# Kernel tuning notes

Measured on AMD Instinct MI355X. Metric: run time of the kernel, lower is better.

The kernel has to match this reference:

```python
import jax, jax.numpy as jnp
import numpy as np

NUM_HEADS = 8


def setup_inputs() -> dict:
    key = jax.random.key(0)
    ks = jax.random.split(key, 7)
    b, t, prompt_dim, emb_dim = 2, 4096, 256, 512
    hidden = emb_dim  # head_dim=None -> hidden_dim = emb_dim
    def xavier(k, fan_in, fan_out):
        limit = np.sqrt(6.0 / (fan_in + fan_out)).astype(np.float32)
        return jax.random.uniform(k, (fan_in, fan_out), jnp.float32, -limit, limit)
    return {
        "prompt": jax.random.normal(ks[0], (b, t, prompt_dim), jnp.float32),
        "Wp": xavier(ks[1], prompt_dim, emb_dim),
        "bp": jnp.zeros((emb_dim,), jnp.float32),
        "Wqkv": xavier(ks[2], emb_dim, 3 * hidden),
        "bqkv": jnp.zeros((3 * hidden,), jnp.float32),
        "Wo": xavier(ks[3], hidden, prompt_dim),
        "bo": jnp.zeros((prompt_dim,), jnp.float32),
    }


def reference(prompt, Wp, bp, Wqkv, bqkv, Wo, bo):
    # prompt_proj
    x = prompt @ Wp + bp                      # [b, t, emb_dim]
    b, t, c = x.shape
    qkv = x @ Wqkv + bqkv                     # [b, t, 3*hidden]
    q, k, v = jnp.split(qkv, 3, axis=2)
    def to_heads(z):
        return z.reshape(b, t, NUM_HEADS, -1).transpose(0, 2, 1, 3)  # [b, h, t, d]
    q, k, v = to_heads(q), to_heads(k), to_heads(v)
    d = k.shape[-1]
    scores = jnp.einsum("bhid,bhjd->bhij", q, k) / jnp.sqrt(jnp.float32(d))
    attn = jax.nn.softmax(scores, axis=-1)    # dropout = identity (eval)
    out = jnp.einsum("bhij,bhjd->bhid", attn, v)
    out = out.transpose(0, 2, 1, 3).reshape(b, t, -1)  # [b, t, hidden]
    return out @ Wo + bo                      # [b, t, prompt_dim]
```

## Files before the change

### kernel.cpp

```cpp
#include <hip/hip_runtime.h>
#include <math.h>
#include <stdint.h>


typedef unsigned short u16;
typedef __attribute__((ext_vector_type(8))) __bf16 bf16x8;
typedef __attribute__((ext_vector_type(4))) __bf16 bf16x4;
typedef __attribute__((ext_vector_type(4))) float f32x4;

#define AS1 __attribute__((address_space(1)))
#define AS3 __attribute__((address_space(3)))

__device__ __forceinline__ void async16(const void* g, void* l) {
  __builtin_amdgcn_global_load_lds((const AS1 void*)g, (AS3 void*)l, 16, 0, 0);
}

__device__ __forceinline__ u16 f2bf(float f) {
  union { float f; unsigned u; } c; c.f = f;
  return (u16)((c.u + 0x7fffu + ((c.u >> 16) & 1u)) >> 16);
}

__global__ void prep_kernel(const float* __restrict__ prompt, u16* __restrict__ pbf,
                            const float* __restrict__ Wp, const float* __restrict__ Wqkv,
                            const float* __restrict__ Wo, u16* __restrict__ woT,
                            const float* __restrict__ bp, const float* __restrict__ bqkv,
                            float* __restrict__ bfused, u16* __restrict__ wfT) {
  __shared__ u16 Asf[64 * 40];
  __shared__ u16 Bsf[64 * 32];
  __shared__ float red[256];
  const int bid = blockIdx.x, tid = threadIdx.x;
  if (bid < 96) {
    const int k0 = (bid & 3) * 64, n0 = (bid >> 2) * 64;
    const int lane = tid & 63, w = tid >> 6;
    const int wr = w >> 1, wc = w & 1;
    const int lr = lane >> 4, lc = lane & 15;
    f32x4 acc[2][2];
#pragma unroll
    for (int a = 0; a < 2; a++)
#pragma unroll
      for (int b = 0; b < 2; b++) acc[a][b] = (f32x4){0.f, 0.f, 0.f, 0.f};
    for (int e0 = 0; e0 < 512; e0 += 32) {
      {
        const int er = tid >> 3, ng = (tid & 7) * 8;
        float4 v1 = *(const float4*)&Wqkv[(e0 + er) * 1536 + n0 + ng];
        float4 v2 = *(const float4*)&Wqkv[(e0 + er) * 1536 + n0 + ng + 4];
        Asf[(ng + 0) * 40 + er] = f2bf(v1.x); Asf[(ng + 1) * 40 + er] = f2bf(v1.y);
        Asf[(ng + 2) * 40 + er] = f2bf(v1.z); Asf[(ng + 3) * 40 + er] = f2bf(v1.w);
        Asf[(ng + 4) * 40 + er] = f2bf(v2.x); Asf[(ng + 5) * 40 + er] = f2bf(v2.y);
        Asf[(ng + 6) * 40 + er] = f2bf(v2.z); Asf[(ng + 7) * 40 + er] = f2bf(v2.w);
      }
      {
        const int kr = tid >> 2, ec = (tid & 3) * 8;
        float4 w1 = *(const float4*)&Wp[(k0 + kr) * 512 + e0 + ec];
        float4 w2 = *(const float4*)&Wp[(k0 + kr) * 512 + e0 + ec + 4];
        u16 tmp[8] = {f2bf(w1.x), f2bf(w1.y), f2bf(w1.z), f2bf(w1.w),
                      f2bf(w2.x), f2bf(w2.y), f2bf(w2.z), f2bf(w2.w)};
        *(uint4*)&Bsf[kr * 32 + ec] = *(const uint4*)&tmp[0];
      }
      __syncthreads();
      bf16x8 af[2], bf2[2];
#pragma unroll
      for (int mi = 0; mi < 2; mi++)
        af[mi] = *(const bf16x8*)&Asf[(wr * 32 + mi * 16 + lc) * 40 + lr * 8];
#pragma unroll
      for (int nj = 0; nj < 2; nj++)
        bf2[nj] = *(const bf16x8*)&Bsf[(wc * 32 + nj * 16 + lc) * 32 + lr * 8];
#pragma unroll
      for (int mi = 0; mi < 2; mi++)
#pragma unroll
        for (int nj = 0; nj < 2; nj++)
          acc[mi][nj] = __builtin_amdgcn_mfma_f32_16x16x32_bf16(af[mi], bf2[nj], acc[mi][nj], 0, 0, 0);
      __syncthreads();
    }
#pragma unroll
    for (int mi = 0; mi < 2; mi++)
#pragma unroll
      for (int nj = 0; nj < 2; nj++)
#pragma unroll
        for (int r = 0; r < 4; r++)
          wfT[(n0 + wr * 32 + mi * 16 + 4 * lr + r) * 256 + k0 + wc * 32 + nj * 16 + lc] =
              f2bf(acc[mi][nj][r]);
  } else if (bid < 120) {
    const int nloc = tid & 63, slice = tid >> 6;
    const int n = (bid - 96) * 64 + nloc;
    float s = 0.f;
#pragma unroll 8
    for (int e = slice * 128; e < slice * 128 + 128; e++) s += bp[e] * Wqkv[e * 1536 + n];
    red[tid] = s;
    __syncthreads();
    if (slice == 0)
      bfused[n] = red[nloc] + red[64 + nloc] + red[128 + nloc] + red[192 + nloc] + bqkv[n];
  } else if (bid < 632) {
    int j = (bid - 120) * 256 + tid;
    int n = j >> 9, k = j & 511;
    woT[j] = f2bf(Wo[k * 256 + n]);
  } else {
    int i = (bid - 632) * 256 + tid;
    float4 v = ((const float4*)prompt)[i];
    ushort4 o;
    o.x = f2bf(v.x); o.y = f2bf(v.y); o.z = f2bf(v.z); o.w = f2bf(v.w);
    ((ushort4*)pbf)[i] = o;
  }
}

__global__ __launch_bounds__(256) void gemm_qkv(
    const u16* __restrict__ A, const u16* __restrict__ Bt, const float* __restrict__ bias,
    u16* __restrict__ qO, u16* __restrict__ kO, u16* __restrict__ vO, int K) {
  constexpr int MI = 4, NJ = 4;
  __shared__ __align__(16) u16 SH[16896];
  const int tid = threadIdx.x;
  const int lane = tid & 63, w = tid >> 6;
  const int wr = w >> 1, wc = w & 1;
  const int lr = lane >> 4, lc = lane & 15;
  const long tileM = (long)blockIdx.y * 128;
  const long tileN = (long)blockIdx.x * 128;

  f32x4 acc[MI][NJ];
#pragma unroll
  for (int a = 0; a < MI; a++)
#pragma unroll
    for (int b = 0; b < NJ; b++) acc[a][b] = (f32x4){0.f, 0.f, 0.f, 0.f};

  const int r0 = lane >> 2;
  const int blk = lane & 3;

  auto stage = [&](int buf, int k0) {
#pragma unroll
    for (int i = 0; i < 2; i++) {
      int r = w * 32 + i * 16 + r0;
      int g = (blk ^ ((r >> 1) & 3)) << 3;
      async16(A + (tileM + r) * (long)K + k0 + g,
              (void*)&SH[buf * 4096 + (w * 32 + i * 16) * 32]);
      async16(Bt + (tileN + r) * (long)K + k0 + g,
              (void*)&SH[8192 + buf * 4096 + (w * 32 + i * 16) * 32]);
    }
  };

  stage(0, 0);
  for (int k0 = 0; k0 < K; k0 += 32) {
    const int cur = (k0 >> 5) & 1;
    stage(cur ^ 1, (k0 + 32 < K) ? k0 + 32 : 0);
    asm volatile("s_waitcnt vmcnt(4)" ::: "memory");
    asm volatile("s_barrier" ::: "memory");

    bf16x8 af[MI], bfv[NJ];
#pragma unroll
    for (int mi = 0; mi < MI; mi++) {
      int r = wr * 64 + mi * 16 + lc;
      af[mi] = *(const bf16x8*)&SH[cur * 4096 + r * 32 + ((lr ^ ((r >> 1) & 3)) << 3)];
    }
#pragma unroll
    for (int nj = 0; nj < NJ; nj++) {
      int r = wc * 64 + nj * 16 + lc;
      bfv[nj] = *(const bf16x8*)&SH[8192 + cur * 4096 + r * 32 + ((lr ^ ((r >> 1) & 3)) << 3)];
    }
#pragma unroll
    for (int mi = 0; mi < MI; mi++)
#pragma unroll
      for (int nj = 0; nj < NJ; nj++)
        acc[mi][nj] = __builtin_amdgcn_mfma_f32_16x16x32_bf16(af[mi], bfv[nj], acc[mi][nj], 0, 0, 0);
    asm volatile("s_barrier" ::: "memory");
  }

  asm volatile("s_waitcnt vmcnt(0)" ::: "memory");
  __syncthreads();

  const int sec = (int)(tileN >> 9);
  const int bb = (int)(tileM >> 12);
  const int t0b = (int)(tileM & 4095);
  const int h0 = ((int)(tileN & 511)) >> 6;
  const float sc = (sec == 0) ? 0.18033688f : 1.f;

#pragma unroll
  for (int mi = 0; mi < MI; mi++)
#pragma unroll
    for (int nj = 0; nj < NJ; nj++) {
      int nloc = wc * 64 + nj * 16 + lc;
      float bcol = bias[tileN + nloc];
      int m0 = wr * 64 + mi * 16 + lr * 4;
      int p0 = m0;
      if (sec == 2) {
        int gg = (m0 >> 2) & 7;
        int posg = ((gg & 3) << 1) | (gg >> 2);
        p0 = (m0 & ~31) | (posg << 2);
      }
      u16 tmp[4];
#pragma unroll
      for (int r = 0; r < 4; r++) tmp[r] = f2bf((acc[mi][nj][r] + bcol) * sc);
      *(uint2*)&SH[nloc * 132 + p0] = *(const uint2*)&tmp[0];
    }
  __syncthreads();

  if (sec == 2) {
    const int rsub = tid >> 4;
    const int cch = tid & 15;
#pragma unroll
    for (int i = 0; i < 8; i++) {
      int row = i * 16 + rsub;
      int hh = row >> 6, d = row & 63;
      bf16x8 vv = *(const bf16x8*)&SH[row * 132 + cch * 8];
      long pl = bb * 8 + h0 + hh;
      *(bf16x8*)&vO[(pl * 64 + d) * 4096 + t0b + cch * 8] = vv;
    }
  } else {
    u16* dst = sec ? kO : qO;
    const int dgrp = lane & 7;
    const int msub = lane >> 3;
#pragma unroll
    for (int hh = 0; hh < 2; hh++) {
      long pl = bb * 8 + h0 + hh;
#pragma unroll
      for (int i = 0; i < 4; i++) {
        int m = w * 8 + msub + i * 32;
        u16 pk[8];
#pragma unroll
        for (int j = 0; j < 8; j++)
          pk[j] = SH[(hh * 64 + dgrp * 8 + j) * 132 + m];
        *(uint4*)&dst[((pl * 4096 + t0b + m) << 6) + dgrp * 8] = *(const uint4*)&pk[0];
      }
    }
  }
}

__global__ __launch_bounds__(512, 4) void flash_attn(
    const u16* __restrict__ Q, const u16* __restrict__ Kg,
    const u16* __restrict__ VTg, u16* __restrict__ Op, float* __restrict__ lp) {
  __shared__ __align__(16) u16 KV[2][8192];

  const int tid = threadIdx.x, lane = tid & 63, w = tid >> 6;
  const int linear = blockIdx.x + 16 * (blockIdx.y + 16 * blockIdx.z);
  const int qt = linear >> 5;
  const int g = linear & 31;
  const int plane = g & 15;
  const int split = g >> 4;
  const int lr = lane >> 4, lc = lane & 15;
  const long pbase = (long)plane << 18;
  const int qr0 = qt * 256 + w * 32;
  const int tj0 = split * 32;

  bf16x8 bq[2][2];
#pragma unroll
  for (int qi = 0; qi < 2; qi++)
#pragma unroll
    for (int kk = 0; kk < 2; kk++)
      bq[qi][kk] = *(const bf16x8*)&Q[pbase + (long)(qr0 + qi * 16 + lc) * 64 + kk * 32 + lr * 8];

  bf16x8 ones;
#pragma unroll
  for (int u = 0; u < 8; u++) ones[u] = (__bf16)1.0f;
  const f32x4 zero4 = (f32x4){0.f, 0.f, 0.f, 0.f};

  f32x4 o[2][4], o1[2];
#pragma unroll
  for (int mi = 0; mi < 2; mi++) {
    o1[mi] = zero4;
#pragma unroll
    for (int nj = 0; nj < 4; nj++) o[mi][nj] = zero4;
  }

  const int krow = lane >> 3, kblk = lane & 7;

  auto stage = [&](int buf, int tj) {
    const u16* kS = Kg + pbase + (long)tj * 4096;
    const u16* vS = VTg + pbase + (long)tj * 64;
    int row = w * 8 + krow;
    async16(kS + (long)row * 64 + ((kblk ^ (row & 7)) << 3),
            (void*)&KV[buf][(w * 8) * 64]);
    async16(vS + (long)row * 4096 + ((kblk ^ (row & 7)) << 3),
            (void*)&KV[buf][4096 + (w * 8) * 64]);
  };

  stage(0, tj0);
  for (int j = 0; j < 32; j++) {
    const int cur = j & 1;
    stage(cur ^ 1, (j + 1 < 32) ? tj0 + j + 1 : tj0);
    asm volatile("s_waitcnt vmcnt(2)" ::: "memory");
    asm volatile("s_barrier" ::: "memory");

    const u16* Ks = &KV[cur][0];
    const u16* Vt = &KV[cur][4096];

    f32x4 s[4][2];
#pragma unroll
    for (int ki = 0; ki < 4; ki++) {
      const int row = ki * 16 + lc;
      bf16x8 ak[2];
#pragma unroll
      for (int kk = 0; kk < 2; kk++)
        ak[kk] = *(const bf16x8*)&Ks[row * 64 + (((kk * 4 + lr) ^ (row & 7)) << 3)];
#pragma unroll
      for (int qi = 0; qi < 2; qi++) {
        s[ki][qi] = __builtin_amdgcn_mfma_f32_16x16x32_bf16(ak[0], bq[qi][0], zero4, 0, 0, 0);
        s[ki][qi] = __builtin_amdgcn_mfma_f32_16x16x32_bf16(ak[1], bq[qi][1], s[ki][qi], 0, 0, 0);
      }
    }

#pragma unroll
    for (int kk = 0; kk < 2; kk++) {
      bf16x8 ap[2];
#pragma unroll
      for (int qi = 0; qi < 2; qi++) {
        bf16x8 p;
#pragma unroll
        for (int r = 0; r < 4; r++) {
          p[r]     = (__bf16)__builtin_amdgcn_exp2f(s[2 * kk][qi][r]);
          p[4 + r] = (__bf16)__builtin_amdgcn_exp2f(s[2 * kk + 1][qi][r]);
        }
        ap[qi] = p;
      }
#pragma unroll
      for (int nj = 0; nj < 4; nj++) {
        const int row = nj * 16 + lc;
        bf16x8 bv = *(const bf16x8*)&Vt[row * 64 + (((kk * 4 + lr) ^ (row & 7)) << 3)];
#pragma unroll
        for (int mi = 0; mi < 2; mi++)
          o[mi][nj] = __builtin_amdgcn_mfma_f32_16x16x32_bf16(ap[mi], bv, o[mi][nj], 0, 0, 0);
      }
#pragma unroll
      for (int mi = 0; mi < 2; mi++)
        o1[mi] = __builtin_amdgcn_mfma_f32_16x16x32_bf16(ap[mi], ones, o1[mi], 0, 0, 0);
    }
    asm volatile("s_barrier" ::: "memory");
  }

  const int bb = plane >> 3, h = plane & 7;
  u16* Ob = Op + (long)split * 4194304;
#pragma unroll
  for (int mi = 0; mi < 2; mi++)
#pragma unroll
    for (int r = 0; r < 4; r++) {
      long t = qr0 + mi * 16 + 4 * lr + r;
#pragma unroll
      for (int nj = 0; nj < 4; nj++)
        Ob[(((long)(bb * 4096 + t) * 8 + h) << 6) + nj * 16 + lc] = f2bf(o[mi][nj][r]);
      if (lc == 0) lp[((split * 16 + plane) << 12) + t] = o1[mi][r];
    }
}

__global__ __launch_bounds__(256) void gemm_out(
    const u16* __restrict__ Op, const float* __restrict__ lp,
    const u16* __restrict__ Bt, const float* __restrict__ bias,
    float* __restrict__ outf) {
  constexpr int K = 512;
  __shared__ __align__(16) u16 As[2][64 * 32];
  __shared__ __align__(16) u16 Bs[2][64 * 32];
  const int tid = threadIdx.x;
  const int lane = tid & 63, w = tid >> 6;
  const int wr = w >> 1, wc = w & 1;
  const int lr = lane >> 4, lc = lane & 15;
  const long tileM = (long)blockIdx.y * 64;
  const long tileN = (long)blockIdx.x * 64;

  f32x4 acc[2][2];
#pragma unroll
  for (int a = 0; a < 2; a++)
#pragma unroll
    for (int b = 0; b < 2; b++) acc[a][b] = (f32x4){0.f, 0.f, 0.f, 0.f};

  const int r0 = lane >> 2;
  const int blk = lane & 3;

  auto stageB = [&](int buf, int k0) {
    int r = w * 16 + r0;
    int g = (blk ^ ((r >> 1) & 3)) << 3;
    async16(Bt + (tileN + r) * (long)K + k0 + g, (void*)&Bs[buf][(w * 16) * 32]);
  };

  const int ar = tid >> 2, ablk = tid & 3;
  const long arow = tileM + ar;
  const int ab = (int)(arow >> 12), at = (int)(arow & 4095);

  auto stageA = [&](int buf, int k0) {
    int h = k0 >> 6;
    float l = lp[(long)((ab * 8 + h) << 12) + at] +
              lp[(long)((16 + ab * 8 + h) << 12) + at];
    float inv = 1.f / l;
    long idx = arow * 512 + k0 + ablk * 8;
    bf16x8 v0 = *(const bf16x8*)&Op[idx];
    bf16x8 v1 = *(const bf16x8*)&Op[4194304 + idx];
    u16 tmp[8];
#pragma unroll
    for (int e = 0; e < 8; e++)
      tmp[e] = f2bf(((float)v0[e] + (float)v1[e]) * inv);
    *(uint4*)&As[buf][ar * 32 + ((ablk ^ ((ar >> 1) & 3)) << 3)] = *(const uint4*)&tmp[0];
  };

  stageB(0, 0);
  for (int k0 = 0; k0 < K; k0 += 32) {
    const int cur = (k0 >> 5) & 1;
    stageB(cur ^ 1, (k0 + 32 < K) ? k0 + 32 : 0);
    stageA(cur, k0);
    asm volatile("s_waitcnt vmcnt(1) lgkmcnt(0)" ::: "memory");
    asm volatile("s_barrier" ::: "memory");

    bf16x8 af[2], bfv[2];
#pragma unroll
    for (int mi = 0; mi < 2; mi++) {
      int r = wr * 32 + mi * 16 + lc;
      af[mi] = *(const bf16x8*)&As[cur][r * 32 + ((lr ^ ((r >> 1) & 3)) << 3)];
    }
#pragma unroll
    for (int nj = 0; nj < 2; nj++) {
      int r = wc * 32 + nj * 16 + lc;
      bfv[nj] = *(const bf16x8*)&Bs[cur][r * 32 + ((lr ^ ((r >> 1) & 3)) << 3)];
    }
#pragma unroll
    for (int mi = 0; mi < 2; mi++)
#pragma unroll
      for (int nj = 0; nj < 2; nj++)
        acc[mi][nj] = __builtin_amdgcn_mfma_f32_16x16x32_bf16(af[mi], bfv[nj], acc[mi][nj], 0, 0, 0);
    asm volatile("s_barrier" ::: "memory");
  }

#pragma unroll
  for (int mi = 0; mi < 2; mi++)
#pragma unroll
    for (int nj = 0; nj < 2; nj++) {
      long col = tileN + wc * 32 + nj * 16 + lc;
      float bcol = bias[col];
      long row0 = tileM + wr * 32 + mi * 16 + lr * 4;
#pragma unroll
      for (int r = 0; r < 4; r++)
        outf[(row0 + r) * 256 + col] = acc[mi][nj][r] + bcol;
    }
}

extern "C" void kernel_launch(void* const* d_in, const int* in_sizes, int n_in,
                              void* d_out, int out_size, void* d_ws, size_t ws_size,
                              hipStream_t stream) {
  const float* prompt = (const float*)d_in[0];
  const float* Wp = (const float*)d_in[1];
  const float* bp = (const float*)d_in[2];
  const float* Wqkv = (const float*)d_in[3];
  const float* bqkv = (const float*)d_in[4];
  const float* Wo = (const float*)d_in[5];
  const float* bo = (const float*)d_in[6];
  float* out = (float*)d_out;

  char* ws = (char*)d_ws;
  const size_t MiB = 1024 * 1024;
  u16* qb     = (u16*)(ws + 0);
  u16* kb     = (u16*)(ws + 8 * MiB);
  u16* vb     = (u16*)(ws + 16 * MiB);
  u16* pbf    = (u16*)(ws + 24 * MiB);
  float* lpp  = (float*)(ws + 24 * MiB);
  u16* Op     = (u16*)(ws + 28 * MiB);
  u16* woT    = (u16*)(ws + 44 * MiB);
  u16* wfT    = (u16*)(ws + 44 * MiB + 256 * 1024);
  float* bfused = (float*)(ws + 45 * MiB);

  prep_kernel<<<dim3(2680), dim3(256), 0, stream>>>(
      prompt, pbf, Wp, Wqkv, Wo, woT, bp, bqkv, bfused, wfT);

  gemm_qkv<<<dim3(12, 64), dim3(256), 0, stream>>>(
      pbf, wfT, bfused, qb, kb, vb, 256);

  flash_attn<<<dim3(16, 16, 2), dim3(512), 0, stream>>>(qb, kb, vb, Op, lpp);

  gemm_out<<<dim3(4, 128), dim3(256), 0, stream>>>(Op, lpp, woT, bo, out);
}
```

Baseline: 176.0 us.

## Fuse prompt bf16 conversion into QKV GEMM and register-prefetch A tiles

Removes the separate prompt fp32-to-bf16 pass from the prep kernel. The QKV GEMM now reads fp32 prompt rows directly into registers, converts them and writes them to LDS one iteration ahead. The output GEMM likewise splits its A staging into a register prefetch (load) and a later convert/write, so global latency overlaps the MFMA work. This cuts a full write and re-read of the bf16 prompt buffer, at the cost of more registers and twice the A-side global bytes inside the GEMM.

```diff
diff --git a/kernel.cpp b/kernel.cpp
--- a/kernel.cpp
+++ b/kernel.cpp
@@ -20,8 +20,7 @@
   return (u16)((c.u + 0x7fffu + ((c.u >> 16) & 1u)) >> 16);
 }
 
-__global__ void prep_kernel(const float* __restrict__ prompt, u16* __restrict__ pbf,
-                            const float* __restrict__ Wp, const float* __restrict__ Wqkv,
+__global__ void prep_kernel(const float* __restrict__ Wp, const float* __restrict__ Wqkv,
                             const float* __restrict__ Wo, u16* __restrict__ woT,
                             const float* __restrict__ bp, const float* __restrict__ bqkv,
                             float* __restrict__ bfused, u16* __restrict__ wfT) {
@@ -90,21 +89,15 @@
     __syncthreads();
     if (slice == 0)
       bfused[n] = red[nloc] + red[64 + nloc] + red[128 + nloc] + red[192 + nloc] + bqkv[n];
-  } else if (bid < 632) {
+  } else {
     int j = (bid - 120) * 256 + tid;
     int n = j >> 9, k = j & 511;
     woT[j] = f2bf(Wo[k * 256 + n]);
-  } else {
-    int i = (bid - 632) * 256 + tid;
-    float4 v = ((const float4*)prompt)[i];
-    ushort4 o;
-    o.x = f2bf(v.x); o.y = f2bf(v.y); o.z = f2bf(v.z); o.w = f2bf(v.w);
-    ((ushort4*)pbf)[i] = o;
   }
 }
 
 __global__ __launch_bounds__(256) void gemm_qkv(
-    const u16* __restrict__ A, const u16* __restrict__ Bt, const float* __restrict__ bias,
+    const float* __restrict__ Ap, const u16* __restrict__ Bt, const float* __restrict__ bias,
     u16* __restrict__ qO, u16* __restrict__ kO, u16* __restrict__ vO, int K) {
   constexpr int MI = 4, NJ = 4;
   __shared__ __align__(16) u16 SH[16896];
@@ -124,23 +117,45 @@
   const int r0 = lane >> 2;
   const int blk = lane & 3;
 
-  auto stage = [&](int buf, int k0) {
+  auto stageB = [&](int buf, int k0) {
 #pragma unroll
     for (int i = 0; i < 2; i++) {
       int r = w * 32 + i * 16 + r0;
       int g = (blk ^ ((r >> 1) & 3)) << 3;
-      async16(A + (tileM + r) * (long)K + k0 + g,
-              (void*)&SH[buf * 4096 + (w * 32 + i * 16) * 32]);
       async16(Bt + (tileN + r) * (long)K + k0 + g,
               (void*)&SH[8192 + buf * 4096 + (w * 32 + i * 16) * 32]);
     }
   };
 
-  stage(0, 0);
+  float4 aLo[2], aHi[2];
+  auto loadA = [&](int k0) {
+#pragma unroll
+    for (int i = 0; i < 2; i++) {
+      int r = w * 32 + i * 16 + r0;
+      int gch = blk ^ ((r >> 1) & 3);
+      const float* src = &Ap[(tileM + r) * 256 + k0 + gch * 8];
+      aLo[i] = *(const float4*)src;
+      aHi[i] = *(const float4*)(src + 4);
+    }
+  };
+  auto writeA = [&](int buf) {
+#pragma unroll
+    for (int i = 0; i < 2; i++) {
+      int r = w * 32 + i * 16 + r0;
+      u16 t[8] = {f2bf(aLo[i].x), f2bf(aLo[i].y), f2bf(aLo[i].z), f2bf(aLo[i].w),
+                  f2bf(aHi[i].x), f2bf(aHi[i].y), f2bf(aHi[i].z), f2bf(aHi[i].w)};
+      *(uint4*)&SH[buf * 4096 + r * 32 + blk * 8] = *(const uint4*)&t[0];
+    }
+  };
+
+  stageB(0, 0);
+  loadA(0);
   for (int k0 = 0; k0 < K; k0 += 32) {
     const int cur = (k0 >> 5) & 1;
-    stage(cur ^ 1, (k0 + 32 < K) ? k0 + 32 : 0);
-    asm volatile("s_waitcnt vmcnt(4)" ::: "memory");
+    stageB(cur ^ 1, (k0 + 32 < K) ? k0 + 32 : 0);
+    writeA(cur);
+    loadA((k0 + 32 < K) ? k0 + 32 : 0);
+    asm volatile("s_waitcnt lgkmcnt(0)" ::: "memory");
     asm volatile("s_barrier" ::: "memory");
 
     bf16x8 af[MI], bfv[NJ];
@@ -370,27 +385,35 @@
   const long arow = tileM + ar;
   const int ab = (int)(arow >> 12), at = (int)(arow & 4095);
 
-  auto stageA = [&](int buf, int k0) {
+  bf16x8 av0, av1;
+  float l0n, l1n;
+
+  auto loadA = [&](int k0) {
     int h = k0 >> 6;
-    float l = lp[(long)((ab * 8 + h) << 12) + at] +
-              lp[(long)((16 + ab * 8 + h) << 12) + at];
-    float inv = 1.f / l;
+    l0n = lp[(long)((ab * 8 + h) << 12) + at];
+    l1n = lp[(long)((16 + ab * 8 + h) << 12) + at];
     long idx = arow * 512 + k0 + ablk * 8;
-    bf16x8 v0 = *(const bf16x8*)&Op[idx];
-    bf16x8 v1 = *(const bf16x8*)&Op[4194304 + idx];
+    av0 = *(const bf16x8*)&Op[idx];
+    av1 = *(const bf16x8*)&Op[4194304 + idx];
+  };
+
+  auto writeA = [&](int buf) {
+    float inv = 1.f / (l0n + l1n);
     u16 tmp[8];
 #pragma unroll
     for (int e = 0; e < 8; e++)
-      tmp[e] = f2bf(((float)v0[e] + (float)v1[e]) * inv);
+      tmp[e] = f2bf(((float)av0[e] + (float)av1[e]) * inv);
     *(uint4*)&As[buf][ar * 32 + ((ablk ^ ((ar >> 1) & 3)) << 3)] = *(const uint4*)&tmp[0];
   };
 
   stageB(0, 0);
+  loadA(0);
   for (int k0 = 0; k0 < K; k0 += 32) {
     const int cur = (k0 >> 5) & 1;
     stageB(cur ^ 1, (k0 + 32 < K) ? k0 + 32 : 0);
-    stageA(cur, k0);
-    asm volatile("s_waitcnt vmcnt(1) lgkmcnt(0)" ::: "memory");
+    writeA(cur);
+    loadA((k0 + 32 < K) ? k0 + 32 : 0);
+    asm volatile("s_waitcnt lgkmcnt(0)" ::: "memory");
     asm volatile("s_barrier" ::: "memory");
 
     bf16x8 af[2], bfv[2];
@@ -442,18 +465,17 @@
   u16* qb     = (u16*)(ws + 0);
   u16* kb     = (u16*)(ws + 8 * MiB);
   u16* vb     = (u16*)(ws + 16 * MiB);
-  u16* pbf    = (u16*)(ws + 24 * MiB);
   float* lpp  = (float*)(ws + 24 * MiB);
   u16* Op     = (u16*)(ws + 28 * MiB);
   u16* woT    = (u16*)(ws + 44 * MiB);
   u16* wfT    = (u16*)(ws + 44 * MiB + 256 * 1024);
   float* bfused = (float*)(ws + 45 * MiB);
 
-  prep_kernel<<<dim3(2680), dim3(256), 0, stream>>>(
-      prompt, pbf, Wp, Wqkv, Wo, woT, bp, bqkv, bfused, wfT);
+  prep_kernel<<<dim3(632), dim3(256), 0, stream>>>(
+      Wp, Wqkv, Wo, woT, bp, bqkv, bfused, wfT);
 
   gemm_qkv<<<dim3(12, 64), dim3(256), 0, stream>>>(
-      pbf, wfT, bfused, qb, kb, vb, 256);
+      prompt, wfT, bfused, qb, kb, vb, 256);
 
   flash_attn<<<dim3(16, 16, 2), dim3(512), 0, stream>>>(qb, kb, vb, Op, lpp);
 
```

Result: no change. 178.9 us (+1.6%).
